# Performance work log

Hardware: AMD Instinct MI355X
Metric: run time of the kernel (lower is better)

Reference implementation:

```python
import jax, jax.numpy as jnp
import numpy as np

EPS = 1e-12  # matches torch F.normalize eps clamp


def _l2norm(v, axis):
    n = jnp.sqrt(jnp.sum(v * v, axis=axis, keepdims=True))
    return v / jnp.maximum(n, EPS)


def setup_inputs() -> dict:
    key = jax.random.key(0)
    k1, k2, k3, k4 = jax.random.split(key, 4)
    N, C, H, W, K = 64, 128, 64, 64, 64
    x = jax.random.normal(k1, (N, C, H, W), dtype=jnp.float32)
    conv_w = jax.random.normal(k2, (K, C), dtype=jnp.float32) * 0.1  # 1x1 conv weight squeezed
    conv_b = jax.random.normal(k3, (K,), dtype=jnp.float32) * 0.1
    centroids = jax.random.uniform(k4, (K, C), dtype=jnp.float32)
    return {"x": x, "conv_w": conv_w, "conv_b": conv_b, "centroids": centroids}


def reference(x, conv_w, conv_b, centroids):
    N, C = x.shape[:2]
    K = centroids.shape[0]
    xf = x.reshape(N, C, -1)                                   # (N, C, P) with P = H*W
    # 1x1 conv == per-pixel linear map over channels
    logits = jnp.einsum('ncp,kc->nkp', xf, conv_w) + conv_b[None, :, None]
    a = jax.nn.softmax(logits, axis=1)                         # soft assignment over clusters
    # vlad[n,k,c] = sum_p a[n,k,p] * (x[n,c,p] - centroids[k,c])
    vlad = jnp.einsum('nkp,ncp->nkc', a, xf) \
        - jnp.sum(a, axis=-1)[:, :, None] * centroids[None]    # (N, K, C)
    vlad = _l2norm(vlad, axis=2)                               # intra-cluster normalization
    vlad = vlad.reshape(N, K * C)
    return _l2norm(vlad, axis=1)
```

## Files before the change

kernel.cpp:

```cpp
#include <hip/hip_runtime.h>
#include <math.h>

#define NNIMG 64
#define CCH 128
#define KK 64
#define PP 4096
#define BSPLIT 16
#define PB 256
#define NCHUNK 32
#define TILE_U32 (PB * 66)

typedef __attribute__((ext_vector_type(8))) short short8;
typedef __attribute__((ext_vector_type(4))) float f32x4;

__device__ __forceinline__ unsigned short bf16_rtne(float f) {
  unsigned u = __float_as_uint(f);
  unsigned r = u + 0x7FFFu + ((u >> 16) & 1u);
  return (unsigned short)(r >> 16);
}
__device__ __forceinline__ float bf16_tof(unsigned short h) {
  return __uint_as_float(((unsigned)h) << 16);
}
__device__ __forceinline__ void lgkm_barrier() {
  __asm__ volatile("s_waitcnt lgkmcnt(0)\n\ts_barrier" ::: "memory");
}
__device__ __forceinline__ void load_to_lds16(const float* g, float* l) {
  __builtin_amdgcn_global_load_lds((const __attribute__((address_space(1))) void*)g,
                                   (__attribute__((address_space(3))) void*)l, 16, 0, 0);
}

template <bool USE_WS>
__global__ __launch_bounds__(256, 2) void netvlad_main(
    const float* __restrict__ x, const float* __restrict__ conv_w,
    const float* __restrict__ conv_b, float* __restrict__ vout,
    float* __restrict__ aout) {
  __shared__ __align__(16) unsigned int tile[TILE_U32];
  __shared__ __align__(16) unsigned char scratch[12288];
  float* xraw = (float*)scratch;
  unsigned short* a_lds = (unsigned short*)scratch;
  float* asum_buf = (float*)(scratch + 10240);

  const int t = threadIdx.x;
  const int lane = t & 63;
  const int wv = t >> 6;
  const int m = lane & 15;
  const int q = lane >> 4;

  const int n = blockIdx.x >> 4;
  const int blk = blockIdx.x & 15;
  const float* xbase = x + (size_t)n * CCH * PP + blk * PB;

  auto issue_dma = [&](int ch, int buf) {
    const int c = ch * 4 + wv;
    load_to_lds16(xbase + (size_t)c * PP + lane * 4, &xraw[buf * 1024 + wv * 256]);
  };

  short8 Whi[4][4];
#pragma unroll
  for (int kt = 0; kt < 4; ++kt)
#pragma unroll
    for (int cs = 0; cs < 4; ++cs) {
      const float* wp = conv_w + (kt * 16 + m) * CCH + cs * 32 + q * 8;
      float4 wa = *(const float4*)wp;
      float4 wb = *(const float4*)(wp + 4);
      float fv[8] = {wa.x, wa.y, wa.z, wa.w, wb.x, wb.y, wb.z, wb.w};
      short8 h;
#pragma unroll
      for (int j = 0; j < 8; ++j) h[j] = (short)bf16_rtne(fv[j]);
      Whi[kt][cs] = h;
    }
  float b_regs[4][4];
#pragma unroll
  for (int kt = 0; kt < 4; ++kt)
#pragma unroll
    for (int r = 0; r < 4; ++r) b_regs[kt][r] = conv_b[kt * 16 + q * 4 + r];
  __asm__ volatile("s_waitcnt vmcnt(0)" ::: "memory");

  issue_dma(0, 0);
  issue_dma(1, 1);
  issue_dma(2, 2);
  const unsigned sel_hi = 0x07060302u;

#pragma unroll 1
  for (int ch = 0; ch < NCHUNK; ++ch) {
    if (ch <= NCHUNK - 3)      __asm__ volatile("s_waitcnt vmcnt(2)" ::: "memory");
    else if (ch == NCHUNK - 2) __asm__ volatile("s_waitcnt vmcnt(1)" ::: "memory");
    else                       __asm__ volatile("s_waitcnt vmcnt(0)" ::: "memory");
    __builtin_amdgcn_s_barrier();
    const int buf = ch % 3;
    const float* xr = &xraw[buf * 1024];
    float x0 = xr[t];
    float x1 = xr[256 + t];
    float x2 = xr[512 + t];
    float x3 = xr[768 + t];
    uint2 w;
    w.x = __builtin_amdgcn_perm(__float_as_uint(x1), __float_as_uint(x0), sel_hi);
    w.y = __builtin_amdgcn_perm(__float_as_uint(x3), __float_as_uint(x2), sel_hi);
    *(uint2*)&tile[t * 66 + 2 * ch] = w;
    __asm__ volatile("s_waitcnt lgkmcnt(0)" ::: "memory");
    __builtin_amdgcn_s_barrier();
    if (ch + 3 < NCHUNK) issue_dma(ch + 3, buf);
  }

  const int pair = wv >> 1;
  const int hw = wv & 1;
  unsigned short* amy = a_lds + pair * (KK * 40);
  const unsigned sel_g2 = (m & 1) ? 0x07060302u : 0x05040100u;

  f32x4 vacc[4][4];
#pragma unroll
  for (int kt = 0; kt < 4; ++kt)
#pragma unroll
    for (int ct = 0; ct < 4; ++ct) vacc[kt][ct] = (f32x4){0.f, 0.f, 0.f, 0.f};
  float asum_acc[16];
#pragma unroll
  for (int i = 0; i < 16; ++i) asum_acc[i] = 0.f;

#pragma unroll 1
  for (int gi = 0; gi < 4; ++gi) {
    const int px0 = (pair + 2 * gi) * 32;
    const int prow = px0 + hw * 16 + m;

    f32x4 acc1[4];
#pragma unroll
    for (int kt = 0; kt < 4; ++kt)
      acc1[kt] = (f32x4){b_regs[kt][0], b_regs[kt][1], b_regs[kt][2], b_regs[kt][3]};
    const unsigned int* pcrow = tile + prow * 66;
#pragma unroll
    for (int cs = 0; cs < 4; ++cs) {
      uint2 u01 = *(const uint2*)&pcrow[16 * cs + 4 * q];
      uint2 u23 = *(const uint2*)&pcrow[16 * cs + 4 * q + 2];
      unsigned hs[4] = {u01.x, u01.y, u23.x, u23.y};
      short8 Bf;
      __builtin_memcpy(&Bf, hs, 16);
#pragma unroll
      for (int kt = 0; kt < 4; ++kt)
        acc1[kt] = __builtin_amdgcn_mfma_f32_16x16x32_bf16(Whi[kt][cs], Bf, acc1[kt], 0, 0, 0);
    }

    float ssum = 0.f;
#pragma unroll
    for (int kt = 0; kt < 4; ++kt)
#pragma unroll
      for (int r = 0; r < 4; ++r) {
        float e = __expf(acc1[kt][r]);
        acc1[kt][r] = e;
        ssum += e;
      }
    ssum += __shfl_xor(ssum, 16, 64);
    ssum += __shfl_xor(ssum, 32, 64);
    float inv = 1.0f / ssum;
#pragma unroll
    for (int kt = 0; kt < 4; ++kt)
#pragma unroll
      for (int r = 0; r < 4; ++r) {
        float a = acc1[kt][r] * inv;
        unsigned short h = bf16_rtne(a);
        asum_acc[kt * 4 + r] += bf16_tof(h);
        amy[(kt * 16 + q * 4 + r) * 40 + hw * 16 + m] = h;
      }
    lgkm_barrier();

    short8 Af[4];
#pragma unroll
    for (int kt = 0; kt < 4; ++kt)
      Af[kt] = *(const short8*)&amy[(kt * 16 + m) * 40 + q * 8];
#pragma unroll
    for (int ct = 0; ct < 4; ++ct) {
      const int ebase = hw * 32 + ct * 8 + (m >> 1);
      unsigned g[8];
#pragma unroll
      for (int j = 0; j < 8; ++j) g[j] = tile[(px0 + q * 8 + j) * 66 + ebase];
      unsigned hs2[4];
#pragma unroll
      for (int i = 0; i < 4; ++i)
        hs2[i] = __builtin_amdgcn_perm(g[2 * i + 1], g[2 * i], sel_g2);
      short8 Bf;
      __builtin_memcpy(&Bf, hs2, 16);
#pragma unroll
      for (int kt = 0; kt < 4; ++kt)
        vacc[kt][ct] = __builtin_amdgcn_mfma_f32_16x16x32_bf16(Af[kt], Bf, vacc[kt][ct], 0, 0, 0);
    }
    lgkm_barrier();
  }

  float* vscr = (float*)tile;
  if (pair == 1) {
#pragma unroll
    for (int kt = 0; kt < 4; ++kt)
#pragma unroll
      for (int ct = 0; ct < 4; ++ct)
#pragma unroll
        for (int r = 0; r < 4; ++r)
          vscr[(kt * 16 + q * 4 + r) * CCH + hw * 64 + ct * 16 + m] = vacc[kt][ct][r];
  }
#pragma unroll
  for (int i = 0; i < 16; ++i) {
    float v = asum_acc[i];
    v += __shfl_xor(v, 1, 64);
    v += __shfl_xor(v, 2, 64);
    v += __shfl_xor(v, 4, 64);
    v += __shfl_xor(v, 8, 64);
    if (m == 0) asum_buf[wv * 64 + (i >> 2) * 16 + q * 4 + (i & 3)] = v;
  }
  lgkm_barrier();
  if (pair == 0) {
    float* vrow = USE_WS ? (vout + (size_t)blockIdx.x * (KK * CCH))
                         : (vout + (size_t)n * (KK * CCH));
#pragma unroll
    for (int kt = 0; kt < 4; ++kt)
#pragma unroll
      for (int ct = 0; ct < 4; ++ct)
#pragma unroll
        for (int r = 0; r < 4; ++r) {
          const int idx = (kt * 16 + q * 4 + r) * CCH + hw * 64 + ct * 16 + m;
          const float v = vacc[kt][ct][r] + vscr[idx];
          if (USE_WS) vrow[idx] = v;
          else atomicAdd(&vrow[idx], v);
        }
  }
  if (t < KK) {
    float s = asum_buf[t] + asum_buf[64 + t] + asum_buf[128 + t] + asum_buf[192 + t];
    if (USE_WS) aout[blockIdx.x * KK + t] = s;
    else atomicAdd(&aout[n * KK + t], s);
  }
}

__global__ __launch_bounds__(256) void netvlad_finish(
    const float* __restrict__ vg, const float* __restrict__ ag,
    const float* __restrict__ centroids, float* __restrict__ out) {
  const int t = threadIdx.x;
  const int w = t >> 6, ln = t & 63;
  const int idx = blockIdx.x * 4 + w;
  const int n = idx >> 6, k = idx & 63;
  const int c = ln * 2;
  float2 v = *(const float2*)&vg[(size_t)(n * KK + k) * CCH + c];
  float s = ag[n * KK + k];
  float2 ce = *(const float2*)&centroids[k * CCH + c];
  float v0 = v.x - s * ce.x;
  float v1 = v.y - s * ce.y;
  float ssq = v0 * v0 + v1 * v1;
#pragma unroll
  for (int off = 32; off > 0; off >>= 1) ssq += __shfl_xor(ssq, off, 64);
  float inv = 0.125f / fmaxf(sqrtf(ssq), 1e-12f);
  float2 o;
  o.x = v0 * inv;
  o.y = v1 * inv;
  *(float2*)&out[(size_t)n * (KK * CCH) + k * CCH + c] = o;
}

__global__ __launch_bounds__(256) void netvlad_finish_ws(
    const float* __restrict__ vp, const float* __restrict__ agp,
    const float* __restrict__ centroids, float* __restrict__ out) {
  const int t = threadIdx.x;
  const int w = t >> 6, ln = t & 63;
  const int idx = blockIdx.x * 4 + w;
  const int n = idx >> 6, k = idx & 63;
  const int c = ln * 2;
  float a0 = 0.f, a1 = 0.f, s = 0.f;
#pragma unroll
  for (int b = 0; b < BSPLIT; ++b) {
    const float* vr = vp + (size_t)(n * BSPLIT + b) * (KK * CCH) + k * CCH + c;
    float2 v = *(const float2*)vr;
    a0 += v.x;
    a1 += v.y;
    s += agp[(n * BSPLIT + b) * KK + k];
  }
  float2 ce = *(const float2*)&centroids[k * CCH + c];
  float v0 = a0 - s * ce.x;
  float v1 = a1 - s * ce.y;
  float ssq = v0 * v0 + v1 * v1;
#pragma unroll
  for (int off = 32; off > 0; off >>= 1) ssq += __shfl_xor(ssq, off, 64);
  float inv = 0.125f / fmaxf(sqrtf(ssq), 1e-12f);
  float2 o;
  o.x = v0 * inv;
  o.y = v1 * inv;
  *(float2*)&out[(size_t)n * (KK * CCH) + k * CCH + c] = o;
}

extern "C" void kernel_launch(void* const* d_in, const int* in_sizes, int n_in,
                              void* d_out, int out_size, void* d_ws, size_t ws_size,
                              hipStream_t stream) {
  const float* x = (const float*)d_in[0];
  const float* conv_w = (const float*)d_in[1];
  const float* conv_b = (const float*)d_in[2];
  const float* centroids = (const float*)d_in[3];
  float* out = (float*)d_out;

  const size_t WS_NEEDED =
      ((size_t)NNIMG * BSPLIT * KK * CCH + (size_t)NNIMG * BSPLIT * KK) * sizeof(float);

  if (ws_size >= WS_NEEDED) {
    float* vp = (float*)d_ws;
    float* agp = vp + (size_t)NNIMG * BSPLIT * KK * CCH;
    netvlad_main<true><<<NNIMG * BSPLIT, 256, 0, stream>>>(x, conv_w, conv_b, vp, agp);
    netvlad_finish_ws<<<NNIMG * KK / 4, 256, 0, stream>>>(vp, agp, centroids, out);
  } else {
    float* vg = (float*)d_ws;
    float* ag = vg + (size_t)NNIMG * KK * CCH;
    const size_t zbytes = ((size_t)NNIMG * KK * CCH + NNIMG * KK) * sizeof(float);
    hipMemsetAsync(d_ws, 0, zbytes, stream);
    netvlad_main<false><<<NNIMG * BSPLIT, 256, 0, stream>>>(x, conv_w, conv_b, vg, ag);
    netvlad_finish<<<NNIMG * KK / 4, 256, 0, stream>>>(vg, ag, centroids, out);
  }
}
```

Before: 242.8 us.

## Stream pixel chunks through double-buffered LDS with register prefetch, two waves

Replaces the up-front transpose of the whole 256-pixel tile (via global_load_lds DMA) with a loop over 32-pixel chunks. Each chunk is prefetched into registers, transposed into one of two small LDS buffers, and consumed immediately by the logits/softmax/VLAD MFMAs. The block shrinks to 128 threads (2 waves), each owning 64 channels, which drops the cross-wave partial VLAD reduction through LDS. LDS use falls sharply, so more blocks can fit per CU. The cost is fewer waves per block, smaller MFMA batches per barrier, and one barrier pair per chunk.

```diff
diff --git a/kernel.cpp b/kernel.cpp
--- a/kernel.cpp
+++ b/kernel.cpp
@@ -7,8 +7,8 @@
 #define PP 4096
 #define BSPLIT 16
 #define PB 256
-#define NCHUNK 32
-#define TILE_U32 (PB * 66)
+#define PC 32
+#define NCHUNK (PB / PC)
 
 typedef __attribute__((ext_vector_type(8))) short short8;
 typedef __attribute__((ext_vector_type(4))) float f32x4;
@@ -24,21 +24,15 @@
 __device__ __forceinline__ void lgkm_barrier() {
   __asm__ volatile("s_waitcnt lgkmcnt(0)\n\ts_barrier" ::: "memory");
 }
-__device__ __forceinline__ void load_to_lds16(const float* g, float* l) {
-  __builtin_amdgcn_global_load_lds((const __attribute__((address_space(1))) void*)g,
-                                   (__attribute__((address_space(3))) void*)l, 16, 0, 0);
-}
 
 template <bool USE_WS>
-__global__ __launch_bounds__(256, 2) void netvlad_main(
+__global__ __launch_bounds__(128, 2) void netvlad_main(
     const float* __restrict__ x, const float* __restrict__ conv_w,
     const float* __restrict__ conv_b, float* __restrict__ vout,
     float* __restrict__ aout) {
-  __shared__ __align__(16) unsigned int tile[TILE_U32];
-  __shared__ __align__(16) unsigned char scratch[12288];
-  float* xraw = (float*)scratch;
-  unsigned short* a_lds = (unsigned short*)scratch;
-  float* asum_buf = (float*)(scratch + 10240);
+  __shared__ __align__(16) unsigned int pc[2][PC * 66];
+  __shared__ __align__(16) unsigned short a_lds[KK * 40];
+  __shared__ float asum_buf[2 * KK];
 
   const int t = threadIdx.x;
   const int lane = t & 63;
@@ -50,10 +44,18 @@
   const int blk = blockIdx.x & 15;
   const float* xbase = x + (size_t)n * CCH * PP + blk * PB;
 
-  auto issue_dma = [&](int ch, int buf) {
-    const int c = ch * 4 + wv;
-    load_to_lds16(xbase + (size_t)c * PP + lane * 4, &xraw[buf * 1024 + wv * 256]);
+  const int lrow = lane >> 3;
+  const int lpx = (lane & 7) * 4;
+  f32x4 sreg[8];
+  auto issue_loads = [&](int ch) {
+#pragma unroll
+    for (int j = 0; j < 8; ++j) {
+      const int row = wv * 64 + (j >> 1) * 16 + lrow * 2 + (j & 1);
+      sreg[j] = *(const f32x4*)(xbase + (size_t)row * PP + ch * PC + lpx);
+    }
   };
+
+  issue_loads(0);
 
   short8 Whi[4][4];
 #pragma unroll
@@ -74,58 +76,42 @@
   for (int kt = 0; kt < 4; ++kt)
 #pragma unroll
     for (int r = 0; r < 4; ++r) b_regs[kt][r] = conv_b[kt * 16 + q * 4 + r];
-  __asm__ volatile("s_waitcnt vmcnt(0)" ::: "memory");
-
-  issue_dma(0, 0);
-  issue_dma(1, 1);
-  issue_dma(2, 2);
+
+  f32x4 vacc[4][4];
+#pragma unroll
+  for (int kt = 0; kt < 4; ++kt)
+#pragma unroll
+    for (int ct = 0; ct < 4; ++ct) vacc[kt][ct] = (f32x4){0.f, 0.f, 0.f, 0.f};
+  float asum_acc[16];
+#pragma unroll
+  for (int i = 0; i < 16; ++i) asum_acc[i] = 0.f;
+
+  const int prow = wv * 16 + m;
   const unsigned sel_hi = 0x07060302u;
+  const unsigned sel_g2 = (m & 1) ? 0x07060302u : 0x05040100u;
 
 #pragma unroll 1
   for (int ch = 0; ch < NCHUNK; ++ch) {
-    if (ch <= NCHUNK - 3)      __asm__ volatile("s_waitcnt vmcnt(2)" ::: "memory");
-    else if (ch == NCHUNK - 2) __asm__ volatile("s_waitcnt vmcnt(1)" ::: "memory");
-    else                       __asm__ volatile("s_waitcnt vmcnt(0)" ::: "memory");
-    __builtin_amdgcn_s_barrier();
-    const int buf = ch % 3;
-    const float* xr = &xraw[buf * 1024];
-    float x0 = xr[t];
-    float x1 = xr[256 + t];
-    float x2 = xr[512 + t];
-    float x3 = xr[768 + t];
-    uint2 w;
-    w.x = __builtin_amdgcn_perm(__float_as_uint(x1), __float_as_uint(x0), sel_hi);
-    w.y = __builtin_amdgcn_perm(__float_as_uint(x3), __float_as_uint(x2), sel_hi);
-    *(uint2*)&tile[t * 66 + 2 * ch] = w;
-    __asm__ volatile("s_waitcnt lgkmcnt(0)" ::: "memory");
-    __builtin_amdgcn_s_barrier();
-    if (ch + 3 < NCHUNK) issue_dma(ch + 3, buf);
-  }
-
-  const int pair = wv >> 1;
-  const int hw = wv & 1;
-  unsigned short* amy = a_lds + pair * (KK * 40);
-  const unsigned sel_g2 = (m & 1) ? 0x07060302u : 0x05040100u;
-
-  f32x4 vacc[4][4];
-#pragma unroll
-  for (int kt = 0; kt < 4; ++kt)
-#pragma unroll
-    for (int ct = 0; ct < 4; ++ct) vacc[kt][ct] = (f32x4){0.f, 0.f, 0.f, 0.f};
-  float asum_acc[16];
-#pragma unroll
-  for (int i = 0; i < 16; ++i) asum_acc[i] = 0.f;
-
-#pragma unroll 1
-  for (int gi = 0; gi < 4; ++gi) {
-    const int px0 = (pair + 2 * gi) * 32;
-    const int prow = px0 + hw * 16 + m;
+    unsigned int* pcb = pc[ch & 1];
+
+#pragma unroll
+    for (int u = 0; u < 4; ++u) {
+      const int e = wv * 32 + u * 8 + lrow;
+      f32x4 ev = sreg[2 * u];
+      f32x4 od = sreg[2 * u + 1];
+#pragma unroll
+      for (int pi = 0; pi < 4; ++pi)
+        pcb[(lpx + pi) * 66 + e] =
+            __builtin_amdgcn_perm(__float_as_uint(od[pi]), __float_as_uint(ev[pi]), sel_hi);
+    }
+    if (ch + 1 < NCHUNK) issue_loads(ch + 1);
+    lgkm_barrier();
 
     f32x4 acc1[4];
 #pragma unroll
     for (int kt = 0; kt < 4; ++kt)
       acc1[kt] = (f32x4){b_regs[kt][0], b_regs[kt][1], b_regs[kt][2], b_regs[kt][3]};
-    const unsigned int* pcrow = tile + prow * 66;
+    const unsigned int* pcrow = pcb + prow * 66;
 #pragma unroll
     for (int cs = 0; cs < 4; ++cs) {
       uint2 u01 = *(const uint2*)&pcrow[16 * cs + 4 * q];
@@ -157,20 +143,20 @@
         float a = acc1[kt][r] * inv;
         unsigned short h = bf16_rtne(a);
         asum_acc[kt * 4 + r] += bf16_tof(h);
-        amy[(kt * 16 + q * 4 + r) * 40 + hw * 16 + m] = h;
+        a_lds[(kt * 16 + q * 4 + r) * 40 + prow] = h;
       }
     lgkm_barrier();
 
     short8 Af[4];
 #pragma unroll
     for (int kt = 0; kt < 4; ++kt)
-      Af[kt] = *(const short8*)&amy[(kt * 16 + m) * 40 + q * 8];
+      Af[kt] = *(const short8*)&a_lds[(kt * 16 + m) * 40 + q * 8];
 #pragma unroll
     for (int ct = 0; ct < 4; ++ct) {
-      const int ebase = hw * 32 + ct * 8 + (m >> 1);
+      const int ebase = wv * 32 + ct * 8 + (m >> 1);
       unsigned g[8];
 #pragma unroll
-      for (int j = 0; j < 8; ++j) g[j] = tile[(px0 + q * 8 + j) * 66 + ebase];
+      for (int j = 0; j < 8; ++j) g[j] = pcb[(q * 8 + j) * 66 + ebase];
       unsigned hs2[4];
 #pragma unroll
       for (int i = 0; i < 4; ++i)
@@ -181,19 +167,20 @@
       for (int kt = 0; kt < 4; ++kt)
         vacc[kt][ct] = __builtin_amdgcn_mfma_f32_16x16x32_bf16(Af[kt], Bf, vacc[kt][ct], 0, 0, 0);
     }
-    lgkm_barrier();
-  }
-
-  float* vscr = (float*)tile;
-  if (pair == 1) {
-#pragma unroll
-    for (int kt = 0; kt < 4; ++kt)
-#pragma unroll
-      for (int ct = 0; ct < 4; ++ct)
-#pragma unroll
-        for (int r = 0; r < 4; ++r)
-          vscr[(kt * 16 + q * 4 + r) * CCH + hw * 64 + ct * 16 + m] = vacc[kt][ct][r];
-  }
+  }
+
+  float* vrow = USE_WS ? (vout + (size_t)blockIdx.x * (KK * CCH))
+                       : (vout + (size_t)n * (KK * CCH));
+#pragma unroll
+  for (int kt = 0; kt < 4; ++kt)
+#pragma unroll
+    for (int ct = 0; ct < 4; ++ct)
+#pragma unroll
+      for (int r = 0; r < 4; ++r) {
+        const int idx = (kt * 16 + q * 4 + r) * CCH + wv * 64 + ct * 16 + m;
+        if (USE_WS) vrow[idx] = vacc[kt][ct][r];
+        else atomicAdd(&vrow[idx], vacc[kt][ct][r]);
+      }
 #pragma unroll
   for (int i = 0; i < 16; ++i) {
     float v = asum_acc[i];
@@ -204,23 +191,8 @@
     if (m == 0) asum_buf[wv * 64 + (i >> 2) * 16 + q * 4 + (i & 3)] = v;
   }
   lgkm_barrier();
-  if (pair == 0) {
-    float* vrow = USE_WS ? (vout + (size_t)blockIdx.x * (KK * CCH))
-                         : (vout + (size_t)n * (KK * CCH));
-#pragma unroll
-    for (int kt = 0; kt < 4; ++kt)
-#pragma unroll
-      for (int ct = 0; ct < 4; ++ct)
-#pragma unroll
-        for (int r = 0; r < 4; ++r) {
-          const int idx = (kt * 16 + q * 4 + r) * CCH + hw * 64 + ct * 16 + m;
-          const float v = vacc[kt][ct][r] + vscr[idx];
-          if (USE_WS) vrow[idx] = v;
-          else atomicAdd(&vrow[idx], v);
-        }
-  }
   if (t < KK) {
-    float s = asum_buf[t] + asum_buf[64 + t] + asum_buf[128 + t] + asum_buf[192 + t];
+    float s = asum_buf[t] + asum_buf[KK + t];
     if (USE_WS) aout[blockIdx.x * KK + t] = s;
     else atomicAdd(&aout[n * KK + t], s);
   }
@@ -294,14 +266,14 @@
   if (ws_size >= WS_NEEDED) {
     float* vp = (float*)d_ws;
     float* agp = vp + (size_t)NNIMG * BSPLIT * KK * CCH;
-    netvlad_main<true><<<NNIMG * BSPLIT, 256, 0, stream>>>(x, conv_w, conv_b, vp, agp);
+    netvlad_main<true><<<NNIMG * BSPLIT, 128, 0, stream>>>(x, conv_w, conv_b, vp, agp);
     netvlad_finish_ws<<<NNIMG * KK / 4, 256, 0, stream>>>(vp, agp, centroids, out);
   } else {
     float* vg = (float*)d_ws;
     float* ag = vg + (size_t)NNIMG * KK * CCH;
     const size_t zbytes = ((size_t)NNIMG * KK * CCH + NNIMG * KK) * sizeof(float);
     hipMemsetAsync(d_ws, 0, zbytes, stream);
-    netvlad_main<false><<<NNIMG * BSPLIT, 256, 0, stream>>>(x, conv_w, conv_b, vg, ag);
+    netvlad_main<false><<<NNIMG * BSPLIT, 128, 0, stream>>>(x, conv_w, conv_b, vg, ag);
     netvlad_finish<<<NNIMG * KK / 4, 256, 0, stream>>>(vg, ag, centroids, out);
   }
 }
```

New measurement: 217.2 us. -10.5%, faster.
